# Optimization experiments

Measured on AMD Instinct MI355X. Metric: run time of the kernel, lower is better.

Reference implementation:

```python
import jax, jax.numpy as jnp
import numpy as np

B, T, D = 2, 1024, 1024
NUM_HEADS_ARG = 16
HS = D // NUM_HEADS_ARG          # 64 (per-head size)
H = HS                           # bug in source: num_heads passed = head_size -> 64 heads
FF = 4 * D
EPS = 1e-5


def _layernorm(x, gamma, beta):
    mu = jnp.mean(x, axis=-1, keepdims=True)
    var = jnp.mean(jnp.square(x - mu), axis=-1, keepdims=True)
    return (x - mu) * jax.lax.rsqrt(var + EPS) * gamma + beta


def setup_inputs() -> dict:
    key = jax.random.key(0)
    ks = jax.random.split(key, 12)
    s_d = 1.0 / np.sqrt(D)
    s_cat = 1.0 / np.sqrt(H * HS)
    s_ff = 1.0 / np.sqrt(FF)
    return {
        "x": jax.random.normal(ks[0], (B, T, D), jnp.float32),
        "Wq": jax.random.uniform(ks[1], (H, D, HS), jnp.float32, -s_d, s_d),
        "Wk": jax.random.uniform(ks[2], (H, D, HS), jnp.float32, -s_d, s_d),
        "Wv": jax.random.uniform(ks[3], (H, D, HS), jnp.float32, -s_d, s_d),
        "Wo": jax.random.uniform(ks[4], (H * HS, D), jnp.float32, -s_cat, s_cat),
        "bo": jax.random.uniform(ks[5], (D,), jnp.float32, -s_cat, s_cat),
        "W1": jax.random.uniform(ks[6], (D, FF), jnp.float32, -s_d, s_d),
        "b1": jax.random.uniform(ks[7], (FF,), jnp.float32, -s_d, s_d),
        "W2": jax.random.uniform(ks[8], (FF, D), jnp.float32, -s_ff, s_ff),
        "b2": jax.random.uniform(ks[9], (D,), jnp.float32, -s_ff, s_ff),
        "g1": jnp.ones((D,), jnp.float32),
        "be1": jnp.zeros((D,), jnp.float32),
        "g2": jnp.ones((D,), jnp.float32),
        "be2": jnp.zeros((D,), jnp.float32),
    }


def reference(x, Wq, Wk, Wv, Wo, bo, W1, b1, W2, b2, g1, be1, g2, be2):
    # per-head projections (no bias): [B,H,T,hs]
    q = jnp.einsum('btd,hde->bhte', x, Wq)
    k = jnp.einsum('btd,hde->bhte', x, Wk)
    v = jnp.einsum('btd,hde->bhte', x, Wv)
    scores = jnp.einsum('bhte,bhse->bhts', q, k) / np.sqrt(HS)  # [B,H,T,T]
    causal = jnp.tril(jnp.ones((T, T), bool))
    scores = jnp.where(causal, scores, -jnp.inf)
    probs = jax.nn.softmax(scores, axis=-1)
    att = jnp.einsum('bhts,bhse->bhte', probs, v)               # [B,H,T,hs]
    # torch stack(dim=3) -> [B,T,hs,H] then flatten: index = d*H + h
    cat = jnp.transpose(att, (0, 2, 3, 1)).reshape(B, T, HS * H)
    mha = cat @ Wo + bo
    x1 = _layernorm(x + mha, g1, be1)
    ff = jax.nn.relu(x1 @ W1 + b1) @ W2 + b2
    return _layernorm(x1 + ff, g2, be2)
```

## Files before the change

### kernel.cpp

```cpp
#include <hip/hip_runtime.h>

typedef unsigned short u16;
typedef __bf16 bf16x8 __attribute__((ext_vector_type(8)));
typedef float f32x4 __attribute__((ext_vector_type(4)));

#define B_ 2
#define T_ 1024
#define D_ 1024
#define H_ 64
#define HS_ 64
#define FF_ 4096
#define SZ_QKV 8388608L
#define S_SCALE 0.1803368801111f

__device__ __forceinline__ float bf2f(u16 u) {
  union { unsigned int v; float f; } x; x.v = ((unsigned int)u) << 16; return x.f;
}
__device__ __forceinline__ u16 f2bf(float f) {
  union { float f; unsigned int v; } x; x.f = f;
  unsigned int r = x.v + 0x7fffu + ((x.v >> 16) & 1u);
  return (u16)(r >> 16);
}
__device__ __forceinline__ u16 f2bf_rtz(float f) {
  union { float f; unsigned int v; } x; x.f = f;
  return (u16)(x.v >> 16);
}

typedef __attribute__((address_space(3))) unsigned int lds_u32;
typedef __attribute__((address_space(1))) const unsigned int glb_u32;
__device__ __forceinline__ void gload_lds16(const void* g, void* l) {
  __builtin_amdgcn_global_load_lds((glb_u32*)g, (lds_u32*)l, 16, 0, 0);
}

__global__ __launch_bounds__(256) void prep(
    const float* __restrict__ x, const float* __restrict__ Wq,
    const float* __restrict__ Wk, const float* __restrict__ Wv,
    const float* __restrict__ Wo, const float* __restrict__ W1,
    const float* __restrict__ W2,
    u16* __restrict__ xb, u16* __restrict__ Wqkvt, u16* __restrict__ Wot,
    u16* __restrict__ W1t, u16* __restrict__ W2t)
{
  __shared__ float tile[64][65];
  int id = blockIdx.x;
  if (id < 1024) {
    const long i = ((long)id * 256 + threadIdx.x) * 8;
    float4 a = *(const float4*)(x + i);
    float4 b = *(const float4*)(x + i + 4);
    union { uint4 v; u16 u[8]; } o;
    o.u[0]=f2bf(a.x); o.u[1]=f2bf(a.y); o.u[2]=f2bf(a.z); o.u[3]=f2bf(a.w);
    o.u[4]=f2bf(b.x); o.u[5]=f2bf(b.y); o.u[6]=f2bf(b.z); o.u[7]=f2bf(b.w);
    *(uint4*)(xb + i) = o.v;
    return;
  }
  id -= 1024;
  const float* in; u16* out; long ibase, obase; int in_rs, out_rs, r0, c0;
  if (id < 3072) {
    const int w = id >> 10, rem = id & 1023;
    const int z = rem >> 4, rt = rem & 15;
    in = (w == 0) ? Wq : (w == 1) ? Wk : Wv;
    ibase = (long)z * 65536; in_rs = 64; r0 = rt * 64; c0 = 0;
    out = Wqkvt + (long)w * 4194304;
    obase = (long)z * 65536; out_rs = 1024;
  } else if (id < 4096) {
    const int rem = id - 3072;
    const int z = rem >> 4, ct = rem & 15;
    in = Wo; ibase = (long)z * 1024; in_rs = 65536; r0 = 0; c0 = ct * 64;
    out = Wot; obase = (long)z * 64; out_rs = 4096;
  } else if (id < 5120) {
    const int rem = id - 4096;
    const int rt = rem >> 6, ct = rem & 63;
    in = W1; ibase = 0; in_rs = 4096; r0 = rt * 64; c0 = ct * 64;
    out = W1t; obase = 0; out_rs = 1024;
  } else {
    const int rem = id - 5120;
    const int rt = rem >> 4, ct = rem & 15;
    in = W2; ibase = 0; in_rs = 1024; r0 = rt * 64; c0 = ct * 64;
    out = W2t; obase = 0; out_rs = 4096;
  }
  const int t = threadIdx.x, lr = t >> 4, lc4 = (t & 15) * 4;
  #pragma unroll
  for (int j = 0; j < 4; ++j) {
    float4 f = *(const float4*)(in + ibase + (long)(r0 + lr + j * 16) * in_rs + c0 + lc4);
    tile[lr + j * 16][lc4]     = f.x;
    tile[lr + j * 16][lc4 + 1] = f.y;
    tile[lr + j * 16][lc4 + 2] = f.z;
    tile[lr + j * 16][lc4 + 3] = f.w;
  }
  __syncthreads();
  const int cr = t >> 3, ch = t & 7;
  #pragma unroll
  for (int j2 = 0; j2 < 2; ++j2) {
    const int crr = cr + j2 * 32;
    union { uint4 v; u16 u[8]; } o;
    #pragma unroll
    for (int i = 0; i < 8; ++i) o.u[i] = f2bf(tile[ch * 8 + i][crr]);
    *(uint4*)(out + obase + (long)(c0 + crr) * out_rs + r0 + ch * 8) = o.v;
  }
}

template<int EPI, int LDA, int LDB>
__global__ __launch_bounds__(512, 2) void gemm8(
    const u16* __restrict__ A, const u16* __restrict__ Bt, u16* __restrict__ C,
    const float* __restrict__ bias, int K, int koff, int ldc)
{
  __shared__ __attribute__((aligned(16))) u16 As[3][256 * 64];
  __shared__ __attribute__((aligned(16))) u16 Bs[3][128 * 64];
  const int bm = blockIdx.x, bn = blockIdx.y, bz = blockIdx.z;
  const long ko = (long)bz * koff;
  const int tid = threadIdx.x, wave = tid >> 6, lane = tid & 63;
  const int quad = lane >> 4, l16 = lane & 15;
  const int wm = (wave >> 1) * 64;
  const int wn = (wave & 1) * 64;
  const int slog = ((tid & 7) ^ ((tid >> 3) & 7)) * 8;
  const int srow = tid >> 3;
  const int ph0 = ((quad)     ^ (l16 & 7)) * 8;
  const int ph1 = ((4 + quad) ^ (l16 & 7)) * 8;

  const u16* Ag = A + (long)(bm * 256) * LDA + ko + slog;
  const u16* Bg = Bt + (long)(bn * 128) * LDB + ko + slog;

  f32x4 acc[4][4];
  #pragma unroll
  for (int i = 0; i < 4; ++i)
    #pragma unroll
    for (int j = 0; j < 4; ++j) acc[i][j] = (f32x4){0.f, 0.f, 0.f, 0.f};

  const int nK = K >> 6;

  auto STAGE_A = [&](int d, int t, int half) {
    const int kk = t << 6;
    gload_lds16(Ag + (long)(half * 128 + srow) * LDA + kk,
                (u16*)As[d] + (half * 1024 + tid) * 8);
    gload_lds16(Ag + (long)(half * 128 + 64 + srow) * LDA + kk,
                (u16*)As[d] + (half * 1024 + 512 + tid) * 8);
  };
  auto STAGE_B = [&](int d, int t) {
    const int kk = t << 6;
    gload_lds16(Bg + (long)(srow) * LDB + kk, (u16*)Bs[d] + tid * 8);
    gload_lds16(Bg + (long)(64 + srow) * LDB + kk, (u16*)Bs[d] + (512 + tid) * 8);
  };

  STAGE_A(0, 0, 0); STAGE_A(0, 0, 1); STAGE_B(0, 0);
  STAGE_A(1, 1, 0); STAGE_A(1, 1, 1); STAGE_B(1, 1);

  bf16x8 a0[2][2], b0[2][2], b1[2][2];
  int cur = 0;
  for (int t = 0; t < nK; ++t) {
    const int nxt = (cur >= 1) ? cur - 1 : cur + 2;
    const bool st = (t + 2) < nK;
    const u16* Ab = As[cur];
    const u16* Bb = Bs[cur];

    if (t < nK - 1) { asm volatile("s_waitcnt vmcnt(6)" ::: "memory"); }
    else            { asm volatile("s_waitcnt vmcnt(0)" ::: "memory"); }
    __builtin_amdgcn_sched_barrier(0);
    __builtin_amdgcn_s_barrier();
    __builtin_amdgcn_sched_barrier(0);
    #pragma unroll
    for (int ii = 0; ii < 2; ++ii) {
      const u16* r = Ab + (wm + ii * 16 + l16) * 64;
      a0[ii][0] = *(const bf16x8*)(r + ph0);
      a0[ii][1] = *(const bf16x8*)(r + ph1);
    }
    #pragma unroll
    for (int jj = 0; jj < 2; ++jj) {
      const u16* r = Bb + (wn + jj * 16 + l16) * 64;
      b0[jj][0] = *(const bf16x8*)(r + ph0);
      b0[jj][1] = *(const bf16x8*)(r + ph1);
    }
    asm volatile("s_waitcnt lgkmcnt(0)" ::: "memory");
    __builtin_amdgcn_sched_barrier(0);
    __builtin_amdgcn_s_setprio(1);
    #pragma unroll
    for (int ii = 0; ii < 2; ++ii)
      #pragma unroll
      for (int jj = 0; jj < 2; ++jj) {
        acc[ii][jj] = __builtin_amdgcn_mfma_f32_16x16x32_bf16(a0[ii][0], b0[jj][0], acc[ii][jj], 0, 0, 0);
        acc[ii][jj] = __builtin_amdgcn_mfma_f32_16x16x32_bf16(a0[ii][1], b0[jj][1], acc[ii][jj], 0, 0, 0);
      }
    __builtin_amdgcn_s_setprio(0);
    __builtin_amdgcn_sched_barrier(0);
    __builtin_amdgcn_s_barrier();

    #pragma unroll
    for (int jj = 0; jj < 2; ++jj) {
      const u16* r = Bb + (wn + (2 + jj) * 16 + l16) * 64;
      b1[jj][0] = *(const bf16x8*)(r + ph0);
      b1[jj][1] = *(const bf16x8*)(r + ph1);
    }
    if (st) STAGE_A(nxt, t + 2, 0);
    __builtin_amdgcn_s_barrier();
    asm volatile("s_waitcnt lgkmcnt(0)" ::: "memory");
    __builtin_amdgcn_sched_barrier(0);
    __builtin_amdgcn_s_setprio(1);
    #pragma unroll
    for (int ii = 0; ii < 2; ++ii)
      #pragma unroll
      for (int jj = 0; jj < 2; ++jj) {
        acc[ii][2 + jj] = __builtin_amdgcn_mfma_f32_16x16x32_bf16(a0[ii][0], b1[jj][0], acc[ii][2 + jj], 0, 0, 0);
        acc[ii][2 + jj] = __builtin_amdgcn_mfma_f32_16x16x32_bf16(a0[ii][1], b1[jj][1], acc[ii][2 + jj], 0, 0, 0);
      }
    __builtin_amdgcn_s_setprio(0);
    __builtin_amdgcn_sched_barrier(0);
    __builtin_amdgcn_s_barrier();

    #pragma unroll
    for (int ii = 0; ii < 2; ++ii) {
      const u16* r = Ab + (wm + (2 + ii) * 16 + l16) * 64;
      a0[ii][0] = *(const bf16x8*)(r + ph0);
      a0[ii][1] = *(const bf16x8*)(r + ph1);
    }
    if (st) STAGE_A(nxt, t + 2, 1);
    __builtin_amdgcn_s_barrier();
    asm volatile("s_waitcnt lgkmcnt(0)" ::: "memory");
    __builtin_amdgcn_sched_barrier(0);
    __builtin_amdgcn_s_setprio(1);
    #pragma unroll
    for (int ii = 0; ii < 2; ++ii)
      #pragma unroll
      for (int jj = 0; jj < 2; ++jj) {
        acc[2 + ii][jj] = __builtin_amdgcn_mfma_f32_16x16x32_bf16(a0[ii][0], b0[jj][0], acc[2 + ii][jj], 0, 0, 0);
        acc[2 + ii][jj] = __builtin_amdgcn_mfma_f32_16x16x32_bf16(a0[ii][1], b0[jj][1], acc[2 + ii][jj], 0, 0, 0);
      }
    __builtin_amdgcn_s_setprio(0);
    __builtin_amdgcn_sched_barrier(0);
    __builtin_amdgcn_s_barrier();

    if (st) STAGE_B(nxt, t + 2);
    __builtin_amdgcn_s_barrier();
    __builtin_amdgcn_s_setprio(1);
    #pragma unroll
    for (int ii = 0; ii < 2; ++ii)
      #pragma unroll
      for (int jj = 0; jj < 2; ++jj) {
        acc[2 + ii][2 + jj] = __builtin_amdgcn_mfma_f32_16x16x32_bf16(a0[ii][0], b1[jj][0], acc[2 + ii][2 + jj], 0, 0, 0);
        acc[2 + ii][2 + jj] = __builtin_amdgcn_mfma_f32_16x16x32_bf16(a0[ii][1], b1[jj][1], acc[2 + ii][2 + jj], 0, 0, 0);
      }
    __builtin_amdgcn_s_setprio(0);
    __builtin_amdgcn_sched_barrier(0);
    __builtin_amdgcn_s_barrier();

    cur = (cur == 2) ? 0 : cur + 1;
  }

  #pragma unroll
  for (int j = 0; j < 4; ++j) {
    const int col = bn * 128 + wn + j * 16 + l16;
    const float bval = (EPI == 1) ? bias[col] : 0.f;
    #pragma unroll
    for (int i = 0; i < 4; ++i) {
      #pragma unroll
      for (int r = 0; r < 4; ++r) {
        const int row = bm * 256 + wm + i * 16 + quad * 4 + r;
        float vv = acc[i][j][r] + bval;
        if (EPI == 1) vv = fmaxf(vv, 0.f);
        if (EPI == 2) {
          const int which = col >> 12, rem = col & 4095;
          const int h = rem >> 6, e = rem & 63;
          const int bb = row >> 10, tt = row & 1023;
          C[(long)which * SZ_QKV + ((long)((bb << 6) + h)) * 65536L + tt * 64 + e] = f2bf(vv);
        } else if (EPI == 3) {
          ((float*)C)[(long)bz * 2097152 + (long)row * ldc + col] = vv;
        } else {
          C[(long)row * ldc + col] = f2bf(vv);
        }
      }
    }
  }
}

__global__ __launch_bounds__(256) void attn_flash(
    const u16* __restrict__ Q, const u16* __restrict__ Kg,
    const u16* __restrict__ V, u16* __restrict__ Om)
{
  __shared__ __attribute__((aligned(16))) u16 Ks[2][64][72];
  __shared__ __attribute__((aligned(16))) u16 Vs[2][64][72];
  __shared__ __attribute__((aligned(16))) u16 QP[4][16][72];
  const int bh = blockIdx.x;
  const int qt = gridDim.y - 1 - blockIdx.y;
  const int b = bh >> 6, h = bh & 63;
  const long base = (long)bh * (T_ * HS_);
  const int tid = threadIdx.x;
  const int wave = tid >> 6, lane = tid & 63, quad = lane >> 4, l16 = lane & 15;
  const int sm = tid >> 2, sc = (tid & 3) * 16;
  const int vswz = (sc >> 4) << 3;

  {
    const int qr = lane >> 3, qe = (lane & 7) * 8;
    #pragma unroll
    for (int j = 0; j < 2; ++j) {
      union { uint4 v; u16 u[8]; } a, o;
      a.v = *(const uint4*)(Q + base + (long)(qt * 64 + wave * 16 + qr + j * 8) * HS_ + qe);
      #pragma unroll
      for (int i = 0; i < 8; ++i) o.u[i] = f2bf(bf2f(a.u[i]) * S_SCALE);
      *(uint4*)&QP[wave][qr + j * 8][qe] = o.v;
    }
  }
  bf16x8 aq0 = *(const bf16x8*)&QP[wave][l16][quad * 8];
  bf16x8 aq1 = *(const bf16x8*)&QP[wave][l16][32 + quad * 8];

  float psum[4] = { 0.f, 0.f, 0.f, 0.f };
  f32x4 oacc[4] = { {0,0,0,0}, {0,0,0,0}, {0,0,0,0}, {0,0,0,0} };

  uint4 kA, kB, vA, vB;
  kA = *(const uint4*)(Kg + base + (long)sm * HS_ + sc);
  kB = *(const uint4*)(Kg + base + (long)sm * HS_ + sc + 8);
  vA = *(const uint4*)(V  + base + (long)sm * HS_ + sc);
  vB = *(const uint4*)(V  + base + (long)sm * HS_ + sc + 8);
  {
    *(uint4*)&Ks[0][sm][sc] = kA; *(uint4*)&Ks[0][sm][sc + 8] = kB;
    union { uint4 v; u16 u[8]; } t0, t1; t0.v = vA; t1.v = vB;
    #pragma unroll
    for (int i = 0; i < 8; ++i) Vs[0][sc + i][sm ^ vswz] = t0.u[i];
    #pragma unroll
    for (int i = 0; i < 8; ++i) Vs[0][sc + 8 + i][sm ^ vswz] = t1.u[i];
  }
  __syncthreads();

  for (int kt = 0; kt <= qt; ++kt) {
    const int cur = kt & 1;
    const bool pf = (kt < qt);
    if (pf) {
      const long nb = base + (long)((kt + 1) * 64 + sm) * HS_ + sc;
      kA = *(const uint4*)(Kg + nb); kB = *(const uint4*)(Kg + nb + 8);
      vA = *(const uint4*)(V  + nb); vB = *(const uint4*)(V  + nb + 8);
    }

    f32x4 sacc[4] = { {0,0,0,0}, {0,0,0,0}, {0,0,0,0}, {0,0,0,0} };
    #pragma unroll
    for (int nt = 0; nt < 4; ++nt) {
      bf16x8 b0 = *(const bf16x8*)&Ks[cur][nt * 16 + l16][quad * 8];
      bf16x8 b1 = *(const bf16x8*)&Ks[cur][nt * 16 + l16][32 + quad * 8];
      sacc[nt] = __builtin_amdgcn_mfma_f32_16x16x32_bf16(aq0, b0, sacc[nt], 0, 0, 0);
      sacc[nt] = __builtin_amdgcn_mfma_f32_16x16x32_bf16(aq1, b1, sacc[nt], 0, 0, 0);
    }

    if (kt == qt) {
      #pragma unroll
      for (int nt = 0; nt < 4; ++nt) {
        const int col = nt * 16 + l16;
        #pragma unroll
        for (int r = 0; r < 4; ++r) {
          const int row = wave * 16 + quad * 4 + r;
          float p = exp2f(sacc[nt][r]);
          p = (col <= row) ? p : 0.f;
          sacc[nt][r] = p; psum[r] += p;
        }
      }
    } else {
      #pragma unroll
      for (int nt = 0; nt < 4; ++nt)
        #pragma unroll
        for (int r = 0; r < 4; ++r) {
          const float p = exp2f(sacc[nt][r]);
          sacc[nt][r] = p; psum[r] += p;
        }
    }

    #pragma unroll
    for (int nt = 0; nt < 4; ++nt)
      #pragma unroll
      for (int r = 0; r < 4; ++r)
        QP[wave][quad * 4 + r][nt * 16 + l16] = f2bf_rtz(sacc[nt][r]);
    bf16x8 p0 = *(const bf16x8*)&QP[wave][l16][quad * 8];
    bf16x8 p1 = *(const bf16x8*)&QP[wave][l16][32 + quad * 8];

    #pragma unroll
    for (int et = 0; et < 4; ++et) {
      const int c0 = ((quad ^ et) * 8);
      bf16x8 b0 = *(const bf16x8*)&Vs[cur][et * 16 + l16][c0];
      bf16x8 b1 = *(const bf16x8*)&Vs[cur][et * 16 + l16][32 + c0];
      oacc[et] = __builtin_amdgcn_mfma_f32_16x16x32_bf16(p0, b0, oacc[et], 0, 0, 0);
      oacc[et] = __builtin_amdgcn_mfma_f32_16x16x32_bf16(p1, b1, oacc[et], 0, 0, 0);
    }

    if (pf) {
      const int nxt = 1 - cur;
      *(uint4*)&Ks[nxt][sm][sc] = kA; *(uint4*)&Ks[nxt][sm][sc + 8] = kB;
      union { uint4 v; u16 u[8]; } t0, t1; t0.v = vA; t1.v = vB;
      #pragma unroll
      for (int i = 0; i < 8; ++i) Vs[nxt][sc + i][sm ^ vswz] = t0.u[i];
      #pragma unroll
      for (int i = 0; i < 8; ++i) Vs[nxt][sc + 8 + i][sm ^ vswz] = t1.u[i];
    }
    __syncthreads();
  }

  #pragma unroll
  for (int off = 1; off < 16; off <<= 1)
    #pragma unroll
    for (int r = 0; r < 4; ++r)
      psum[r] += __shfl_xor(psum[r], off, 64);
  u16 (*Os)[72] = Ks[0];
  #pragma unroll
  for (int r = 0; r < 4; ++r) {
    const float rinv = 1.f / fmaxf(psum[r], 1e-20f);
    const int row = wave * 16 + quad * 4 + r;
    #pragma unroll
    for (int et = 0; et < 4; ++et)
      Os[row][et * 16 + l16] = f2bf(oacc[et][r] * rinv);
  }
  const int orow = wave * 16 + (lane >> 3), oe = (lane & 7) * 8;
  #pragma unroll
  for (int it = 0; it < 2; ++it) {
    const int rr = orow + it * 8;
    uint4 o = *(const uint4*)&Os[rr][oe];
    *(uint4*)(Om + ((long)(b * T_ + qt * 64 + rr)) * 4096 + h * 64 + oe) = o;
  }
}

template<int XBF, int OBF>
__global__ __launch_bounds__(256) void ln_sum4(
    const float* __restrict__ P4, const float* __restrict__ bias,
    const void* __restrict__ Xv, const float* __restrict__ g,
    const float* __restrict__ be, void* __restrict__ outv)
{
  __shared__ float red[8];
  const int row = blockIdx.x, tid = threadIdx.x;
  const long base = (long)row * D_;
  float v4[4]; float s = 0.f;
  #pragma unroll
  for (int j = 0; j < 4; ++j) {
    const int i = tid + j * 256;
    float acc = bias[i];
    #pragma unroll
    for (int p = 0; p < 4; ++p) acc += P4[(long)p * 2097152 + base + i];
    const float xval = XBF ? bf2f(((const u16*)Xv)[base + i]) : ((const float*)Xv)[base + i];
    v4[j] = xval + acc;
    s += v4[j];
  }
  #pragma unroll
  for (int off = 32; off > 0; off >>= 1) s += __shfl_down(s, off, 64);
  if ((tid & 63) == 0) red[tid >> 6] = s;
  __syncthreads();
  const float mu = (red[0] + red[1] + red[2] + red[3]) * (1.f / D_);
  float vs = 0.f;
  #pragma unroll
  for (int j = 0; j < 4; ++j) { const float d = v4[j] - mu; vs += d * d; }
  #pragma unroll
  for (int off = 32; off > 0; off >>= 1) vs += __shfl_down(vs, off, 64);
  __syncthreads();
  if ((tid & 63) == 0) red[tid >> 6] = vs;
  __syncthreads();
  const float rs = rsqrtf((red[0] + red[1] + red[2] + red[3]) * (1.f / D_) + 1e-5f);
  #pragma unroll
  for (int j = 0; j < 4; ++j) {
    const int i = tid + j * 256;
    const float o = (v4[j] - mu) * rs * g[i] + be[i];
    if (OBF) ((u16*)outv)[base + i] = f2bf(o);
    else     ((float*)outv)[base + i] = o;
  }
}

extern "C" void kernel_launch(void* const* d_in, const int* in_sizes, int n_in,
                              void* d_out, int out_size, void* d_ws, size_t ws_size,
                              hipStream_t stream) {
  const float* x   = (const float*)d_in[0];
  const float* Wq  = (const float*)d_in[1];
  const float* Wk  = (const float*)d_in[2];
  const float* Wv  = (const float*)d_in[3];
  const float* Wo  = (const float*)d_in[4];
  const float* bo  = (const float*)d_in[5];
  const float* W1  = (const float*)d_in[6];
  const float* b1  = (const float*)d_in[7];
  const float* W2  = (const float*)d_in[8];
  const float* b2  = (const float*)d_in[9];
  const float* g1  = (const float*)d_in[10];
  const float* be1 = (const float*)d_in[11];
  const float* g2  = (const float*)d_in[12];
  const float* be2 = (const float*)d_in[13];
  float* out = (float*)d_out;

  u16* ws = (u16*)d_ws;
  u16* xb    = ws;
  u16* Wqkvt = xb + 2097152;
  u16* Wot   = Wqkvt + 12582912;
  u16* W1t   = Wot + 4194304;
  u16* W2t   = W1t + 4194304;
  u16* q     = W2t + 4194304;
  u16* k     = q + SZ_QKV;
  u16* v     = k + SZ_QKV;
  u16* Om    = v + SZ_QKV;
  float* P1 = (float*)q;
  float* P2 = (float*)q;
  u16* x1  = v;
  u16* h1  = Om;

  dim3 blk(256);
  dim3 blk8(512);

  prep<<<dim3(7168), blk, 0, stream>>>(x, Wq, Wk, Wv, Wo, W1, W2,
                                       xb, Wqkvt, Wot, W1t, W2t);

  gemm8<2, 1024, 1024><<<dim3(8, 96), blk8, 0, stream>>>(
      xb, Wqkvt, q, nullptr, 1024, 0, 0);

  attn_flash<<<dim3(128, 16), blk, 0, stream>>>(q, k, v, Om);

  gemm8<3, 4096, 4096><<<dim3(8, 8, 4), blk8, 0, stream>>>(
      Om, Wot, (u16*)P1, nullptr, 1024, 1024, 1024);

  ln_sum4<0, 1><<<dim3(2048), blk, 0, stream>>>(P1, bo, x, g1, be1, x1);

  gemm8<1, 1024, 1024><<<dim3(8, 32), blk8, 0, stream>>>(
      x1, W1t, h1, b1, 1024, 0, 4096);

  gemm8<3, 4096, 4096><<<dim3(8, 8, 4), blk8, 0, stream>>>(
      h1, W2t, (u16*)P2, nullptr, 1024, 1024, 1024);

  ln_sum4<1, 0><<<dim3(2048), blk, 0, stream>>>(P2, b2, x1, g2, be2, out);

  (void)in_sizes; (void)n_in; (void)out_size; (void)ws_size;
}
```

Measured before the change: 387.9 us.

## Remap GEMM blocks across XCDs and drop intra-iteration barriers in pipeline

Replaces the 2D/3D GEMM grid with a flat grid whose block index is remapped so that consecutive tiles land on the same XCD, aiming for better L2 reuse of shared A/B panels. The main loop drops most of the per-quarter s_barriers and explicit lgkmcnt waits. It now issues global-to-LDS prefetch chunks interleaved with each MFMA quarter, with register fragments held in full 4x2 arrays. This is meant to cut synchronization stalls and overlap the next-stage loads with compute. In exchange, correctness now rests on a single top-of-loop barrier to protect the triple-buffered LDS, and register use rises.

```diff
diff --git a/kernel.cpp b/kernel.cpp
--- a/kernel.cpp
+++ b/kernel.cpp
@@ -99,13 +99,16 @@
 }
 
 template<int EPI, int LDA, int LDB>
-__global__ __launch_bounds__(512, 2) void gemm8(
+__global__ __launch_bounds__(512, 2) void gemm8b(
     const u16* __restrict__ A, const u16* __restrict__ Bt, u16* __restrict__ C,
     const float* __restrict__ bias, int K, int koff, int ldc)
 {
   __shared__ __attribute__((aligned(16))) u16 As[3][256 * 64];
   __shared__ __attribute__((aligned(16))) u16 Bs[3][128 * 64];
-  const int bm = blockIdx.x, bn = blockIdx.y, bz = blockIdx.z;
+  const int nwg = gridDim.x, cpx = nwg >> 3;
+  const int sid = (blockIdx.x & 7) * cpx + (blockIdx.x >> 3);
+  const int bm = sid & 7, bn = sid >> 3;
+  const int bz = blockIdx.z;
   const long ko = (long)bz * koff;
   const int tid = threadIdx.x, wave = tid >> 6, lane = tid & 63;
   const int quad = lane >> 4, l16 = lane & 15;
@@ -127,23 +130,23 @@
 
   const int nK = K >> 6;
 
-  auto STAGE_A = [&](int d, int t, int half) {
-    const int kk = t << 6;
-    gload_lds16(Ag + (long)(half * 128 + srow) * LDA + kk,
-                (u16*)As[d] + (half * 1024 + tid) * 8);
-    gload_lds16(Ag + (long)(half * 128 + 64 + srow) * LDA + kk,
-                (u16*)As[d] + (half * 1024 + 512 + tid) * 8);
+  auto STAGE_A = [&](int d, int t, int a) {
+    gload_lds16(Ag + (long)(a * 64 + srow) * LDA + (t << 6),
+                (u16*)As[d] + a * 4096 + tid * 8);
   };
-  auto STAGE_B = [&](int d, int t) {
-    const int kk = t << 6;
-    gload_lds16(Bg + (long)(srow) * LDB + kk, (u16*)Bs[d] + tid * 8);
-    gload_lds16(Bg + (long)(64 + srow) * LDB + kk, (u16*)Bs[d] + (512 + tid) * 8);
+  auto STAGE_B = [&](int d, int t, int b) {
+    gload_lds16(Bg + (long)(b * 64 + srow) * LDB + (t << 6),
+                (u16*)Bs[d] + b * 4096 + tid * 8);
   };
 
-  STAGE_A(0, 0, 0); STAGE_A(0, 0, 1); STAGE_B(0, 0);
-  STAGE_A(1, 1, 0); STAGE_A(1, 1, 1); STAGE_B(1, 1);
-
-  bf16x8 a0[2][2], b0[2][2], b1[2][2];
+  #pragma unroll
+  for (int a = 0; a < 4; ++a) STAGE_A(0, 0, a);
+  STAGE_B(0, 0, 0); STAGE_B(0, 0, 1);
+  #pragma unroll
+  for (int a = 0; a < 4; ++a) STAGE_A(1, 1, a);
+  STAGE_B(1, 1, 0); STAGE_B(1, 1, 1);
+
+  bf16x8 af[4][2], bf[4][2];
   int cur = 0;
   for (int t = 0; t < nK; ++t) {
     const int nxt = (cur >= 1) ? cur - 1 : cur + 2;
@@ -156,91 +159,81 @@
     __builtin_amdgcn_sched_barrier(0);
     __builtin_amdgcn_s_barrier();
     __builtin_amdgcn_sched_barrier(0);
+
     #pragma unroll
     for (int ii = 0; ii < 2; ++ii) {
       const u16* r = Ab + (wm + ii * 16 + l16) * 64;
-      a0[ii][0] = *(const bf16x8*)(r + ph0);
-      a0[ii][1] = *(const bf16x8*)(r + ph1);
+      af[ii][0] = *(const bf16x8*)(r + ph0);
+      af[ii][1] = *(const bf16x8*)(r + ph1);
     }
     #pragma unroll
     for (int jj = 0; jj < 2; ++jj) {
       const u16* r = Bb + (wn + jj * 16 + l16) * 64;
-      b0[jj][0] = *(const bf16x8*)(r + ph0);
-      b0[jj][1] = *(const bf16x8*)(r + ph1);
-    }
-    asm volatile("s_waitcnt lgkmcnt(0)" ::: "memory");
+      bf[jj][0] = *(const bf16x8*)(r + ph0);
+      bf[jj][1] = *(const bf16x8*)(r + ph1);
+    }
+    if (st) { STAGE_A(nxt, t + 2, 0); STAGE_A(nxt, t + 2, 1); }
     __builtin_amdgcn_sched_barrier(0);
     __builtin_amdgcn_s_setprio(1);
     #pragma unroll
     for (int ii = 0; ii < 2; ++ii)
       #pragma unroll
       for (int jj = 0; jj < 2; ++jj) {
-        acc[ii][jj] = __builtin_amdgcn_mfma_f32_16x16x32_bf16(a0[ii][0], b0[jj][0], acc[ii][jj], 0, 0, 0);
-        acc[ii][jj] = __builtin_amdgcn_mfma_f32_16x16x32_bf16(a0[ii][1], b0[jj][1], acc[ii][jj], 0, 0, 0);
+        acc[ii][jj] = __builtin_amdgcn_mfma_f32_16x16x32_bf16(af[ii][0], bf[jj][0], acc[ii][jj], 0, 0, 0);
+        acc[ii][jj] = __builtin_amdgcn_mfma_f32_16x16x32_bf16(af[ii][1], bf[jj][1], acc[ii][jj], 0, 0, 0);
       }
     __builtin_amdgcn_s_setprio(0);
     __builtin_amdgcn_sched_barrier(0);
-    __builtin_amdgcn_s_barrier();
 
     #pragma unroll
     for (int jj = 0; jj < 2; ++jj) {
       const u16* r = Bb + (wn + (2 + jj) * 16 + l16) * 64;
-      b1[jj][0] = *(const bf16x8*)(r + ph0);
-      b1[jj][1] = *(const bf16x8*)(r + ph1);
-    }
-    if (st) STAGE_A(nxt, t + 2, 0);
-    __builtin_amdgcn_s_barrier();
-    asm volatile("s_waitcnt lgkmcnt(0)" ::: "memory");
+      bf[2 + jj][0] = *(const bf16x8*)(r + ph0);
+      bf[2 + jj][1] = *(const bf16x8*)(r + ph1);
+    }
+    if (st) { STAGE_A(nxt, t + 2, 2); STAGE_A(nxt, t + 2, 3); }
     __builtin_amdgcn_sched_barrier(0);
     __builtin_amdgcn_s_setprio(1);
     #pragma unroll
     for (int ii = 0; ii < 2; ++ii)
       #pragma unroll
       for (int jj = 0; jj < 2; ++jj) {
-        acc[ii][2 + jj] = __builtin_amdgcn_mfma_f32_16x16x32_bf16(a0[ii][0], b1[jj][0], acc[ii][2 + jj], 0, 0, 0);
-        acc[ii][2 + jj] = __builtin_amdgcn_mfma_f32_16x16x32_bf16(a0[ii][1], b1[jj][1], acc[ii][2 + jj], 0, 0, 0);
+        acc[ii][2 + jj] = __builtin_amdgcn_mfma_f32_16x16x32_bf16(af[ii][0], bf[2 + jj][0], acc[ii][2 + jj], 0, 0, 0);
+        acc[ii][2 + jj] = __builtin_amdgcn_mfma_f32_16x16x32_bf16(af[ii][1], bf[2 + jj][1], acc[ii][2 + jj], 0, 0, 0);
       }
     __builtin_amdgcn_s_setprio(0);
     __builtin_amdgcn_sched_barrier(0);
-    __builtin_amdgcn_s_barrier();
 
     #pragma unroll
     for (int ii = 0; ii < 2; ++ii) {
       const u16* r = Ab + (wm + (2 + ii) * 16 + l16) * 64;
-      a0[ii][0] = *(const bf16x8*)(r + ph0);
-      a0[ii][1] = *(const bf16x8*)(r + ph1);
-    }
-    if (st) STAGE_A(nxt, t + 2, 1);
-    __builtin_amdgcn_s_barrier();
-    asm volatile("s_waitcnt lgkmcnt(0)" ::: "memory");
+      af[2 + ii][0] = *(const bf16x8*)(r + ph0);
+      af[2 + ii][1] = *(const bf16x8*)(r + ph1);
+    }
+    if (st) { STAGE_B(nxt, t + 2, 0); STAGE_B(nxt, t + 2, 1); }
     __builtin_amdgcn_sched_barrier(0);
     __builtin_amdgcn_s_setprio(1);
     #pragma unroll
     for (int ii = 0; ii < 2; ++ii)
       #pragma unroll
       for (int jj = 0; jj < 2; ++jj) {
-        acc[2 + ii][jj] = __builtin_amdgcn_mfma_f32_16x16x32_bf16(a0[ii][0], b0[jj][0], acc[2 + ii][jj], 0, 0, 0);
-        acc[2 + ii][jj] = __builtin_amdgcn_mfma_f32_16x16x32_bf16(a0[ii][1], b0[jj][1], acc[2 + ii][jj], 0, 0, 0);
+        acc[2 + ii][jj] = __builtin_amdgcn_mfma_f32_16x16x32_bf16(af[2 + ii][0], bf[jj][0], acc[2 + ii][jj], 0, 0, 0);
+        acc[2 + ii][jj] = __builtin_amdgcn_mfma_f32_16x16x32_bf16(af[2 + ii][1], bf[jj][1], acc[2 + ii][jj], 0, 0, 0);
       }
     __builtin_amdgcn_s_setprio(0);
     __builtin_amdgcn_sched_barrier(0);
-    __builtin_amdgcn_s_barrier();
-
-    if (st) STAGE_B(nxt, t + 2);
-    __builtin_amdgcn_s_barrier();
+
     __builtin_amdgcn_s_setprio(1);
     #pragma unroll
     for (int ii = 0; ii < 2; ++ii)
       #pragma unroll
       for (int jj = 0; jj < 2; ++jj) {
-        acc[2 + ii][2 + jj] = __builtin_amdgcn_mfma_f32_16x16x32_bf16(a0[ii][0], b1[jj][0], acc[2 + ii][2 + jj], 0, 0, 0);
-        acc[2 + ii][2 + jj] = __builtin_amdgcn_mfma_f32_16x16x32_bf16(a0[ii][1], b1[jj][1], acc[2 + ii][2 + jj], 0, 0, 0);
+        acc[2 + ii][2 + jj] = __builtin_amdgcn_mfma_f32_16x16x32_bf16(af[2 + ii][0], bf[2 + jj][0], acc[2 + ii][2 + jj], 0, 0, 0);
+        acc[2 + ii][2 + jj] = __builtin_amdgcn_mfma_f32_16x16x32_bf16(af[2 + ii][1], bf[2 + jj][1], acc[2 + ii][2 + jj], 0, 0, 0);
       }
     __builtin_amdgcn_s_setprio(0);
-    __builtin_amdgcn_sched_barrier(0);
-    __builtin_amdgcn_s_barrier();
-
-    cur = (cur == 2) ? 0 : cur + 1;
+
+    cur = nxt == 0 ? (cur == 2 ? 0 : cur + 1) : (cur == 2 ? 0 : cur + 1);
   }
 
   #pragma unroll
@@ -492,20 +485,20 @@
   prep<<<dim3(7168), blk, 0, stream>>>(x, Wq, Wk, Wv, Wo, W1, W2,
                                        xb, Wqkvt, Wot, W1t, W2t);
 
-  gemm8<2, 1024, 1024><<<dim3(8, 96), blk8, 0, stream>>>(
+  gemm8b<2, 1024, 1024><<<dim3(768), blk8, 0, stream>>>(
       xb, Wqkvt, q, nullptr, 1024, 0, 0);
 
   attn_flash<<<dim3(128, 16), blk, 0, stream>>>(q, k, v, Om);
 
-  gemm8<3, 4096, 4096><<<dim3(8, 8, 4), blk8, 0, stream>>>(
+  gemm8b<3, 4096, 4096><<<dim3(64, 1, 4), blk8, 0, stream>>>(
       Om, Wot, (u16*)P1, nullptr, 1024, 1024, 1024);
 
   ln_sum4<0, 1><<<dim3(2048), blk, 0, stream>>>(P1, bo, x, g1, be1, x1);
 
-  gemm8<1, 1024, 1024><<<dim3(8, 32), blk8, 0, stream>>>(
+  gemm8b<1, 1024, 1024><<<dim3(256), blk8, 0, stream>>>(
       x1, W1t, h1, b1, 1024, 0, 4096);
 
-  gemm8<3, 4096, 4096><<<dim3(8, 8, 4), blk8, 0, stream>>>(
+  gemm8b<3, 4096, 4096><<<dim3(64, 1, 4), blk8, 0, stream>>>(
       h1, W2t, (u16*)P2, nullptr, 1024, 1024, 1024);
 
   ln_sum4<1, 0><<<dim3(2048), blk, 0, stream>>>(P2, b2, x1, g2, be2, out);
```

Measured after the change: 357.5 us. 7.8% less time.
